# Kernel optimization log

Measured on AMD Instinct MI355X. Metric: run time of the kernel, lower is better.

Reference implementation:

```python
import jax, jax.numpy as jnp
import numpy as np

N, E, H, L, G = 100000, 1000000, 64, 4, 64
D_IN = 2 * H + 3  # edge/coord MLP input: x[row] ++ x[col] ++ rel(3)


def _lin_params(key, fan_in, fan_out):
    kw, kb = jax.random.split(key)
    s = 1.0 / np.sqrt(fan_in)
    w = jax.random.uniform(kw, (fan_in, fan_out), jnp.float32, -s, s)
    b = jax.random.uniform(kb, (fan_out,), jnp.float32, -s, s)
    return w, b


def _stacked(key, fan_in, fan_out, n=L):
    ks = jax.random.split(key, n)
    ws, bs = zip(*[_lin_params(k, fan_in, fan_out) for k in ks])
    return jnp.stack(ws), jnp.stack(bs)


def setup_inputs() -> dict:
    key = jax.random.key(0)
    ks = jax.random.split(key, 16)
    x = jax.random.normal(ks[0], (N, 1), jnp.float32)
    coords = jax.random.normal(ks[1], (N, 3), jnp.float32)
    edge_index = jax.random.randint(ks[2], (2, E), 0, N, jnp.int32)
    batch = jnp.sort(jax.random.randint(ks[3], (N,), 0, G, jnp.int32))
    in_w, in_b = _lin_params(ks[4], 1, H)
    coord_w1, coord_b1 = _stacked(ks[5], D_IN, 2 * H)
    coord_w2, coord_b2 = _stacked(ks[6], 2 * H, 3)
    ew_w, ew_b = _stacked(ks[7], 3, 1)
    cn_scale = jnp.full((L, 1), 0.01, jnp.float32)
    edge_w1, edge_b1 = _stacked(ks[8], D_IN, 2 * H)
    edge_w2, edge_b2 = _stacked(ks[9], 2 * H, H)
    node_w1, node_b1 = _stacked(ks[10], 2 * H, 2 * H)
    node_w2, node_b2 = _stacked(ks[11], 2 * H, H)
    out_w, out_b = _lin_params(ks[12], H, 128)
    return dict(x=x, coords=coords, in_w=in_w, in_b=in_b,
                coord_w1=coord_w1, coord_b1=coord_b1, coord_w2=coord_w2, coord_b2=coord_b2,
                ew_w=ew_w, ew_b=ew_b, cn_scale=cn_scale,
                edge_w1=edge_w1, edge_b1=edge_b1, edge_w2=edge_w2, edge_b2=edge_b2,
                node_w1=node_w1, node_b1=node_b1, node_w2=node_w2, node_b2=node_b2,
                out_w=out_w, out_b=out_b, edge_index=edge_index, batch=batch)


def _layer_norm(h, eps=1e-5):
    mu = jnp.mean(h, -1, keepdims=True)
    var = jnp.var(h, -1, keepdims=True)
    return (h - mu) / jnp.sqrt(var + eps)


def reference(x, coords, in_w, in_b, coord_w1, coord_b1, coord_w2, coord_b2,
              ew_w, ew_b, cn_scale, edge_w1, edge_b1, edge_w2, edge_b2,
              node_w1, node_b1, node_w2, node_b2, out_w, out_b,
              edge_index, batch):
    row, col = edge_index[0], edge_index[1]
    h = x @ in_w + in_b  # [N, H]
    for l in range(L):
        # 1) coord update from OLD coords
        rel = coords[row] - coords[col]                        # [E, 3]
        cin = jnp.concatenate([h[row], h[col], rel], axis=-1)  # [E, 2H+3]
        delta = jax.nn.silu(cin @ coord_w1[l] + coord_b1[l]) @ coord_w2[l] + coord_b2[l]  # [E,3]
        nrm = jnp.maximum(jnp.linalg.norm(delta, axis=-1, keepdims=True), 1e-8)
        delta = delta / nrm * cn_scale[l]                      # CoorsNorm
        delta = delta * jax.nn.sigmoid(rel @ ew_w[l] + ew_b[l])
        coords = coords.at[row].add(delta)
        # 2) edge message / node update from NEW coords
        rel = coords[row] - coords[col]
        ein = jnp.concatenate([h[row], h[col], rel], axis=-1)
        e = jax.nn.silu(jax.nn.silu(ein @ edge_w1[l] + edge_b1[l]) @ edge_w2[l] + edge_b2[l])
        agg = jnp.zeros_like(h).at[row].add(e)                 # scatter-add [N, H]
        nin = jnp.concatenate([h, agg], axis=-1)
        h = h + jax.nn.silu(nin @ node_w1[l] + node_b1[l]) @ node_w2[l] + node_b2[l]
        h = _layer_norm(h)
    # global mean pool
    sums = jax.ops.segment_sum(h, batch, num_segments=G)
    cnts = jax.ops.segment_sum(jnp.ones((h.shape[0], 1), h.dtype), batch, num_segments=G)
    pooled = sums / jnp.maximum(cnts, 1.0)
    out = jax.nn.relu(pooled) @ out_w + out_b                  # [G, 128]
    return out / jnp.maximum(jnp.linalg.norm(out, axis=-1, keepdims=True), 1e-12)
```

## Files before the change

### kernel.cpp

```cpp
#include <hip/hip_runtime.h>
#include <math.h>

#define NN 100000
#define NE 1000000
#define NG 64
#define NL 4
#define NT_E (NE / 32)
#define NT_N (NN / 32)

typedef __attribute__((ext_vector_type(8))) _Float16 f16x8;
typedef __attribute__((ext_vector_type(4))) float f32x4;

#define MFMA16(a, b, c) __builtin_amdgcn_mfma_f32_16x16x32_f16(a, b, c, 0, 0, 0)
#define LOG2E 1.44269504088896340f
__device__ __forceinline__ float fsig_(float x) {
    return __builtin_amdgcn_rcpf(1.0f + __builtin_amdgcn_exp2f(-LOG2E * x));
}
__device__ __forceinline__ float fsilu_(float x) { return x * fsig_(x); }

__global__ void k_init_h(const float* __restrict__ x, const float* __restrict__ in_w,
                         const float* __restrict__ in_b, float* __restrict__ h32,
                         _Float16* __restrict__ h16) {
    int idx = blockIdx.x * blockDim.x + threadIdx.x;
    if (idx >= NN * 64) return;
    int n = idx >> 6, j = idx & 63;
    float v = fmaf(x[n], in_w[j], in_b[j]);
    h32[idx] = v;
    h16[idx] = (_Float16)v;
}

#define SEG0 21504
#define SEG1 21504
#define SEG2 8704
#define SEG3 17408
#define SEG4 8704
#define SEG5 2176
#define SEGTOT (SEG0 + SEG1 + SEG2 + SEG3 + SEG4 + SEG5)
__global__ void k_prep_all(const float* __restrict__ cw1, const float* __restrict__ ew1,
                           const float* __restrict__ ew2, const float* __restrict__ nw1,
                           const float* __restrict__ nw2, const float* __restrict__ cw2,
                           _Float16* __restrict__ cw1T, _Float16* __restrict__ ew1T,
                           _Float16* __restrict__ ew2T, _Float16* __restrict__ nw1T,
                           _Float16* __restrict__ nw2T, _Float16* __restrict__ cw2T) {
    int i = blockIdx.x * blockDim.x + threadIdx.x;
    if (i >= NL * SEGTOT) return;
    int l = i / SEGTOT, r = i - l * SEGTOT;
    const float* src; _Float16* dst; int K, O, SD, j;
    if (r < SEG0) { src = cw1 + (size_t)l * 131 * 128; dst = cw1T + (size_t)l * SEG0; K = 131; O = 128; SD = 168; j = r; }
    else if ((r -= SEG0) < SEG1) { src = ew1 + (size_t)l * 131 * 128; dst = ew1T + (size_t)l * SEG1; K = 131; O = 128; SD = 168; j = r; }
    else if ((r -= SEG1) < SEG2) { src = ew2 + (size_t)l * 128 * 64; dst = ew2T + (size_t)l * SEG2; K = 128; O = 64; SD = 136; j = r; }
    else if ((r -= SEG2) < SEG3) { src = nw1 + (size_t)l * 128 * 128; dst = nw1T + (size_t)l * SEG3; K = 128; O = 128; SD = 136; j = r; }
    else if ((r -= SEG3) < SEG4) { src = nw2 + (size_t)l * 128 * 64; dst = nw2T + (size_t)l * SEG4; K = 128; O = 64; SD = 136; j = r; }
    else {
        r -= SEG4;
        const float* s2 = cw2 + (size_t)l * 128 * 3;
        int o = r / 136, k = r - o * 136;
        cw2T[(size_t)l * SEG5 + r] = (o < 3 && k < 128) ? (_Float16)s2[(size_t)k * 3 + o] : (_Float16)0.0f;
        return;
    }
    int o = j / SD, k = j - o * SD;
    dst[j] = (k < K) ? (_Float16)src[(size_t)k * O + o] : (_Float16)0.0f;
}

__global__ void k_hist(const int* __restrict__ row, int* __restrict__ deg) {
    int e = blockIdx.x * blockDim.x + threadIdx.x;
    if (e < NE) atomicAdd(&deg[row[e]], 1);
}

#define SCB 256
#define SCT 256
#define SCCH ((NN + SCB - 1) / SCB)
__global__ void k_scan_part(const int* __restrict__ deg, int* __restrict__ bsum) {
    __shared__ int red[SCT];
    int b = blockIdx.x;
    int s = b * SCCH, e = min(NN, s + SCCH);
    int sum = 0;
    for (int i = s + threadIdx.x; i < e; i += SCT) sum += deg[i];
    red[threadIdx.x] = sum;
    __syncthreads();
    for (int off = SCT / 2; off > 0; off >>= 1) {
        if (threadIdx.x < off) red[threadIdx.x] += red[threadIdx.x + off];
        __syncthreads();
    }
    if (threadIdx.x == 0) bsum[b] = red[0];
}
__global__ void k_scan_mid(int* __restrict__ bsum) {
    __shared__ int ss[SCB];
    int t = threadIdx.x;
    ss[t] = bsum[t];
    __syncthreads();
    if (t == 0) {
        int run = 0;
        for (int i = 0; i < SCB; ++i) { int v = ss[i]; ss[i] = run; run += v; }
    }
    __syncthreads();
    bsum[t] = ss[t];
}
__global__ void k_scan_fin(const int* __restrict__ deg, const int* __restrict__ bsum,
                           int* __restrict__ rowptr) {
    __shared__ int tsum[SCT];
    int b = blockIdx.x;
    int s = b * SCCH, e = min(NN, s + SCCH);
    const int per = (SCCH + SCT - 1) / SCT;
    int ts = s + threadIdx.x * per;
    int te = min(e, ts + per);
    int sum = 0;
    for (int i = ts; i < te; ++i) sum += deg[i];
    tsum[threadIdx.x] = sum;
    __syncthreads();
    if (threadIdx.x == 0) {
        int run = bsum[b];
        for (int i = 0; i < SCT; ++i) { int v = tsum[i]; tsum[i] = run; run += v; }
    }
    __syncthreads();
    int run = tsum[threadIdx.x];
    for (int i = ts; i < te; ++i) { rowptr[i] = run; run += deg[i]; }
    if (b == 0 && threadIdx.x == 0) rowptr[NN] = NE;
}

__global__ void k_scatter2(const int* __restrict__ row, const int* __restrict__ col,
                           int* __restrict__ pos, int* __restrict__ rowP,
                           int* __restrict__ colP) {
    int e = blockIdx.x * blockDim.x + threadIdx.x;
    if (e < NE) {
        int r = row[e];
        int p = atomicAdd(&pos[r], 1);
        rowP[p] = r;
        colP[p] = col[e];
    }
}

template <int CSR>
__global__ __launch_bounds__(256)
void k_coord3(const _Float16* __restrict__ h16,
              const float* __restrict__ ccur, float* __restrict__ cnext,
              const int* __restrict__ rowP, const int* __restrict__ colP,
              float4* __restrict__ deltas,
              const _Float16* __restrict__ w1T, const float* __restrict__ b1,
              const _Float16* __restrict__ w2T, const float* __restrict__ b2,
              const float* __restrict__ eww, const float* __restrict__ ewb,
              const float* __restrict__ cns) {
    __shared__ __attribute__((aligned(16))) _Float16 cin[32][168];
    __shared__ __attribute__((aligned(16))) _Float16 h1[32][136];
    __shared__ __attribute__((aligned(16))) float pbuf[4][32][17];
    __shared__ float gate[32];
    for (int i = threadIdx.x; i < 32 * 168; i += 256) (&cin[0][0])[i] = (_Float16)0.0f;
    int tid = threadIdx.x;
    int w = tid >> 6, lane = tid & 63, lc = lane & 15, lg = lane >> 4;
    float e0w = eww[0], e1w = eww[1], e2w = eww[2], ebw = ewb[0], sc = cns[0];
    float b20 = b2[0], b21 = b2[1], b22 = b2[2];
    f16x8 bw1[2][5];
#pragma unroll
    for (int ti = 0; ti < 2; ++ti)
#pragma unroll
        for (int ks = 0; ks < 5; ++ks)
            bw1[ti][ks] = *(const f16x8*)&w1T[(size_t)((2 * w + ti) * 16 + lc) * 168 + ks * 32 + lg * 8];
    f16x8 bw2 = *(const f16x8*)&w2T[(size_t)lc * 136 + w * 32 + lg * 8];
    float bias10 = b1[(2 * w) * 16 + lc], bias11 = b1[(2 * w + 1) * 16 + lc];
    __syncthreads();

    for (int tile = blockIdx.x; tile < NT_E; tile += gridDim.x) {
        int e0 = tile * 32;
        {
            int el = tid >> 3, part = tid & 7;
            int r = rowP[e0 + el], c = colP[e0 + el];
            *(f16x8*)&cin[el][part * 8] = *(const f16x8*)&h16[(size_t)r * 64 + part * 8];
            *(f16x8*)&cin[el][64 + part * 8] = *(const f16x8*)&h16[(size_t)c * 64 + part * 8];
        }
        if (tid < 32) {
            int r = rowP[e0 + tid], c = colP[e0 + tid];
            float rx = ccur[r * 3 + 0] - ccur[c * 3 + 0];
            float ry = ccur[r * 3 + 1] - ccur[c * 3 + 1];
            float rz = ccur[r * 3 + 2] - ccur[c * 3 + 2];
            cin[tid][128] = (_Float16)rx; cin[tid][129] = (_Float16)ry; cin[tid][130] = (_Float16)rz;
            gate[tid] = fsig_(fmaf(rx, e0w, fmaf(ry, e1w, fmaf(rz, e2w, ebw))));
        }
        __syncthreads();
        f32x4 acc[2][2];
        acc[0][0] = acc[0][1] = acc[1][0] = acc[1][1] = (f32x4){0.f, 0.f, 0.f, 0.f};
#pragma unroll
        for (int ks = 0; ks < 5; ++ks) {
            f16x8 a0 = *(const f16x8*)&cin[lc][ks * 32 + lg * 8];
            f16x8 a1 = *(const f16x8*)&cin[16 + lc][ks * 32 + lg * 8];
#pragma unroll
            for (int ti = 0; ti < 2; ++ti) {
                acc[0][ti] = MFMA16(a0, bw1[ti][ks], acc[0][ti]);
                acc[1][ti] = MFMA16(a1, bw1[ti][ks], acc[1][ti]);
            }
        }
#pragma unroll
        for (int ti = 0; ti < 2; ++ti) {
            int colc = (2 * w + ti) * 16 + lc;
            float bias = ti ? bias11 : bias10;
#pragma unroll
            for (int rt = 0; rt < 2; ++rt)
#pragma unroll
                for (int j = 0; j < 4; ++j)
                    h1[rt * 16 + lg * 4 + j][colc] = (_Float16)fsilu_(acc[rt][ti][j] + bias);
        }
        __syncthreads();
        f32x4 c2[2];
        c2[0] = c2[1] = (f32x4){0.f, 0.f, 0.f, 0.f};
        {
            f16x8 a0 = *(const f16x8*)&h1[lc][w * 32 + lg * 8];
            f16x8 a1 = *(const f16x8*)&h1[16 + lc][w * 32 + lg * 8];
            c2[0] = MFMA16(a0, bw2, c2[0]);
            c2[1] = MFMA16(a1, bw2, c2[1]);
        }
#pragma unroll
        for (int rt = 0; rt < 2; ++rt)
#pragma unroll
            for (int j = 0; j < 4; ++j)
                pbuf[w][rt * 16 + lg * 4 + j][lc] = c2[rt][j];
        __syncthreads();
        if (tid < 32) {
            float d0 = pbuf[0][tid][0] + pbuf[1][tid][0] + pbuf[2][tid][0] + pbuf[3][tid][0] + b20;
            float d1 = pbuf[0][tid][1] + pbuf[1][tid][1] + pbuf[2][tid][1] + pbuf[3][tid][1] + b21;
            float d2 = pbuf[0][tid][2] + pbuf[1][tid][2] + pbuf[2][tid][2] + pbuf[3][tid][2] + b22;
            float ss = d0 * d0 + d1 * d1 + d2 * d2;
            float nrm = fmaxf(__builtin_amdgcn_sqrtf(ss), 1e-8f);
            float m = sc * __builtin_amdgcn_rcpf(nrm) * gate[tid];
            if (CSR) {
                deltas[e0 + tid] = make_float4(d0 * m, d1 * m, d2 * m, 0.0f);
            } else {
                int r = rowP[e0 + tid];
                atomicAdd(&cnext[(size_t)r * 3 + 0], d0 * m);
                atomicAdd(&cnext[(size_t)r * 3 + 1], d1 * m);
                atomicAdd(&cnext[(size_t)r * 3 + 2], d2 * m);
            }
        }
    }
}

__global__ void k_coord_apply(const float* __restrict__ ccur, float* __restrict__ cnext,
                              const int* __restrict__ rowptr,
                              const float4* __restrict__ deltas) {
    int n = blockIdx.x * blockDim.x + threadIdx.x;
    if (n >= NN) return;
    int s = rowptr[n], e = rowptr[n + 1];
    float d0 = 0.f, d1 = 0.f, d2 = 0.f;
    for (int j = s; j < e; ++j) {
        float4 d = deltas[j];
        d0 += d.x; d1 += d.y; d2 += d.z;
    }
    cnext[(size_t)n * 3 + 0] = ccur[(size_t)n * 3 + 0] + d0;
    cnext[(size_t)n * 3 + 1] = ccur[(size_t)n * 3 + 1] + d1;
    cnext[(size_t)n * 3 + 2] = ccur[(size_t)n * 3 + 2] + d2;
}

template <int CSR>
__global__ __launch_bounds__(256)
void k_edge3(const _Float16* __restrict__ h16, const float* __restrict__ coords,
             float* __restrict__ agg, _Float16* __restrict__ emsgS,
             const int* __restrict__ rowP, const int* __restrict__ colP,
             const _Float16* __restrict__ w1T, const float* __restrict__ b1,
             const _Float16* __restrict__ w2T, const float* __restrict__ b2) {
    __shared__ __attribute__((aligned(16))) _Float16 cin[32][168];
    __shared__ __attribute__((aligned(16))) _Float16 h1[32][136];
    __shared__ __attribute__((aligned(16))) _Float16 msg[32][72];
    for (int i = threadIdx.x; i < 32 * 168; i += 256) (&cin[0][0])[i] = (_Float16)0.0f;
    int tid = threadIdx.x;
    int w = tid >> 6, lane = tid & 63, lc = lane & 15, lg = lane >> 4;
    f16x8 bw1[2][5];
#pragma unroll
    for (int ti = 0; ti < 2; ++ti)
#pragma unroll
        for (int ks = 0; ks < 5; ++ks)
            bw1[ti][ks] = *(const f16x8*)&w1T[(size_t)((2 * w + ti) * 16 + lc) * 168 + ks * 32 + lg * 8];
    f16x8 bw2[4];
#pragma unroll
    for (int ks = 0; ks < 4; ++ks)
        bw2[ks] = *(const f16x8*)&w2T[(size_t)(w * 16 + lc) * 136 + ks * 32 + lg * 8];
    float bias10 = b1[(2 * w) * 16 + lc], bias11 = b1[(2 * w + 1) * 16 + lc];
    float bias2 = b2[w * 16 + lc];
    __syncthreads();

    for (int tile = blockIdx.x; tile < NT_E; tile += gridDim.x) {
        int e0 = tile * 32;
        {
            int el = tid >> 3, part = tid & 7;
            int r = rowP[e0 + el], c = colP[e0 + el];
            *(f16x8*)&cin[el][part * 8] = *(const f16x8*)&h16[(size_t)r * 64 + part * 8];
            *(f16x8*)&cin[el][64 + part * 8] = *(const f16x8*)&h16[(size_t)c * 64 + part * 8];
        }
        if (tid < 32) {
            int r = rowP[e0 + tid], c = colP[e0 + tid];
            cin[tid][128] = (_Float16)(coords[r * 3 + 0] - coords[c * 3 + 0]);
            cin[tid][129] = (_Float16)(coords[r * 3 + 1] - coords[c * 3 + 1]);
            cin[tid][130] = (_Float16)(coords[r * 3 + 2] - coords[c * 3 + 2]);
        }
        __syncthreads();
        f32x4 acc[2][2];
        acc[0][0] = acc[0][1] = acc[1][0] = acc[1][1] = (f32x4){0.f, 0.f, 0.f, 0.f};
#pragma unroll
        for (int ks = 0; ks < 5; ++ks) {
            f16x8 a0 = *(const f16x8*)&cin[lc][ks * 32 + lg * 8];
            f16x8 a1 = *(const f16x8*)&cin[16 + lc][ks * 32 + lg * 8];
#pragma unroll
            for (int ti = 0; ti < 2; ++ti) {
                acc[0][ti] = MFMA16(a0, bw1[ti][ks], acc[0][ti]);
                acc[1][ti] = MFMA16(a1, bw1[ti][ks], acc[1][ti]);
            }
        }
#pragma unroll
        for (int ti = 0; ti < 2; ++ti) {
            int colc = (2 * w + ti) * 16 + lc;
            float bias = ti ? bias11 : bias10;
#pragma unroll
            for (int rt = 0; rt < 2; ++rt)
#pragma unroll
                for (int j = 0; j < 4; ++j)
                    h1[rt * 16 + lg * 4 + j][colc] = (_Float16)fsilu_(acc[rt][ti][j] + bias);
        }
        __syncthreads();
        f32x4 c2[2];
        c2[0] = c2[1] = (f32x4){0.f, 0.f, 0.f, 0.f};
#pragma unroll
        for (int ks = 0; ks < 4; ++ks) {
            f16x8 a0 = *(const f16x8*)&h1[lc][ks * 32 + lg * 8];
            f16x8 a1 = *(const f16x8*)&h1[16 + lc][ks * 32 + lg * 8];
            c2[0] = MFMA16(a0, bw2[ks], c2[0]);
            c2[1] = MFMA16(a1, bw2[ks], c2[1]);
        }
        if (CSR) {
#pragma unroll
            for (int rt = 0; rt < 2; ++rt)
#pragma unroll
                for (int j = 0; j < 4; ++j)
                    msg[rt * 16 + lg * 4 + j][w * 16 + lc] = (_Float16)fsilu_(c2[rt][j] + bias2);
            __syncthreads();
            int r = tid >> 3, part = tid & 7;
            *(f16x8*)&emsgS[(size_t)(e0 + r) * 64 + part * 8] = *(const f16x8*)&msg[r][part * 8];
        } else {
#pragma unroll
            for (int rt = 0; rt < 2; ++rt)
#pragma unroll
                for (int j = 0; j < 4; ++j)
                    atomicAdd(&agg[(size_t)rowP[e0 + rt * 16 + lg * 4 + j] * 64 + w * 16 + lc],
                              fsilu_(c2[rt][j] + bias2));
            __syncthreads();
        }
    }
}

template <int CSR>
__global__ __launch_bounds__(256)
void k_node3(float* __restrict__ h32, _Float16* __restrict__ h16,
             const float* __restrict__ agg, const _Float16* __restrict__ emsgS,
             const int* __restrict__ rowptr,
             const _Float16* __restrict__ w1T, const float* __restrict__ b1,
             const _Float16* __restrict__ w2T, const float* __restrict__ b2) {
    __shared__ __attribute__((aligned(16))) _Float16 cin[32][136];
    __shared__ __attribute__((aligned(16))) _Float16 h1[32][136];
    __shared__ __attribute__((aligned(16))) float vbuf[32][64];
    int tid = threadIdx.x;
    int w = tid >> 6, lane = tid & 63, lc = lane & 15, lg = lane >> 4;
    f16x8 bw1[2][4], bw2[4];
#pragma unroll
    for (int ti = 0; ti < 2; ++ti)
#pragma unroll
        for (int ks = 0; ks < 4; ++ks)
            bw1[ti][ks] = *(const f16x8*)&w1T[(size_t)((2 * w + ti) * 16 + lc) * 136 + ks * 32 + lg * 8];
#pragma unroll
    for (int ks = 0; ks < 4; ++ks)
        bw2[ks] = *(const f16x8*)&w2T[(size_t)(w * 16 + lc) * 136 + ks * 32 + lg * 8];
    float bias10 = b1[(2 * w) * 16 + lc], bias11 = b1[(2 * w + 1) * 16 + lc];
    float bias2 = b2[w * 16 + lc];

    for (int tile = blockIdx.x; tile < NT_N; tile += gridDim.x) {
        int n0 = tile * 32;
        {
            int nl = tid >> 3, part = tid & 7;
            int n = n0 + nl;
            *(f16x8*)&cin[nl][part * 8] = *(const f16x8*)&h16[(size_t)n * 64 + part * 8];
            if (CSR) {
                float a[8] = {0.f, 0.f, 0.f, 0.f, 0.f, 0.f, 0.f, 0.f};
                int s = rowptr[n], e = rowptr[n + 1];
                for (int jj = s; jj < e; ++jj) {
                    f16x8 m = *(const f16x8*)&emsgS[(size_t)jj * 64 + part * 8];
#pragma unroll
                    for (int q = 0; q < 8; ++q) a[q] += (float)m[q];
                }
                f16x8 o;
#pragma unroll
                for (int q = 0; q < 8; ++q) o[q] = (_Float16)a[q];
                *(f16x8*)&cin[nl][64 + part * 8] = o;
            } else {
                f32x4 xx = *(const f32x4*)&agg[(size_t)n * 64 + part * 8];
                f32x4 yy = *(const f32x4*)&agg[(size_t)n * 64 + part * 8 + 4];
                f16x8 o;
                o[0] = (_Float16)xx[0]; o[1] = (_Float16)xx[1]; o[2] = (_Float16)xx[2]; o[3] = (_Float16)xx[3];
                o[4] = (_Float16)yy[0]; o[5] = (_Float16)yy[1]; o[6] = (_Float16)yy[2]; o[7] = (_Float16)yy[3];
                *(f16x8*)&cin[nl][64 + part * 8] = o;
            }
        }
        __syncthreads();
        f32x4 acc[2][2];
        acc[0][0] = acc[0][1] = acc[1][0] = acc[1][1] = (f32x4){0.f, 0.f, 0.f, 0.f};
#pragma unroll
        for (int ks = 0; ks < 4; ++ks) {
            f16x8 a0 = *(const f16x8*)&cin[lc][ks * 32 + lg * 8];
            f16x8 a1 = *(const f16x8*)&cin[16 + lc][ks * 32 + lg * 8];
#pragma unroll
            for (int ti = 0; ti < 2; ++ti) {
                acc[0][ti] = MFMA16(a0, bw1[ti][ks], acc[0][ti]);
                acc[1][ti] = MFMA16(a1, bw1[ti][ks], acc[1][ti]);
            }
        }
#pragma unroll
        for (int ti = 0; ti < 2; ++ti) {
            int colc = (2 * w + ti) * 16 + lc;
            float bias = ti ? bias11 : bias10;
#pragma unroll
            for (int rt = 0; rt < 2; ++rt)
#pragma unroll
                for (int j = 0; j < 4; ++j)
                    h1[rt * 16 + lg * 4 + j][colc] = (_Float16)fsilu_(acc[rt][ti][j] + bias);
        }
        __syncthreads();
        f32x4 c2[2];
        c2[0] = c2[1] = (f32x4){0.f, 0.f, 0.f, 0.f};
#pragma unroll
        for (int ks = 0; ks < 4; ++ks) {
            f16x8 a0 = *(const f16x8*)&h1[lc][ks * 32 + lg * 8];
            f16x8 a1 = *(const f16x8*)&h1[16 + lc][ks * 32 + lg * 8];
            c2[0] = MFMA16(a0, bw2[ks], c2[0]);
            c2[1] = MFMA16(a1, bw2[ks], c2[1]);
        }
#pragma unroll
        for (int rt = 0; rt < 2; ++rt)
#pragma unroll
            for (int j = 0; j < 4; ++j) {
                int rl = rt * 16 + lg * 4 + j, colc = w * 16 + lc;
                vbuf[rl][colc] = h32[(size_t)(n0 + rl) * 64 + colc] + c2[rt][j] + bias2;
            }
        __syncthreads();
        {
            int r = w * 8 + (lane >> 3), sub = lane & 7;
            f32x4 v0 = *(const f32x4*)&vbuf[r][sub * 8];
            f32x4 v1 = *(const f32x4*)&vbuf[r][sub * 8 + 4];
            float s = v0[0] + v0[1] + v0[2] + v0[3] + v1[0] + v1[1] + v1[2] + v1[3];
            float sq = v0[0]*v0[0] + v0[1]*v0[1] + v0[2]*v0[2] + v0[3]*v0[3]
                     + v1[0]*v1[0] + v1[1]*v1[1] + v1[2]*v1[2] + v1[3]*v1[3];
            s += __shfl_xor(s, 1); s += __shfl_xor(s, 2); s += __shfl_xor(s, 4);
            sq += __shfl_xor(sq, 1); sq += __shfl_xor(sq, 2); sq += __shfl_xor(sq, 4);
            float mu = s * (1.0f / 64.0f);
            float var = sq * (1.0f / 64.0f) - mu * mu;
            float rs = __builtin_amdgcn_rcpf(__builtin_amdgcn_sqrtf(var + 1e-5f));
            size_t base = (size_t)(n0 + r) * 64 + sub * 8;
            f32x4 o0, o1; f16x8 oh;
#pragma unroll
            for (int i = 0; i < 4; ++i) {
                o0[i] = (v0[i] - mu) * rs;
                o1[i] = (v1[i] - mu) * rs;
                oh[i] = (_Float16)o0[i];
                oh[4 + i] = (_Float16)o1[i];
            }
            *(f32x4*)&h32[base] = o0;
            *(f32x4*)&h32[base + 4] = o1;
            *(f16x8*)&h16[base] = oh;
        }
        __syncthreads();
    }
}

__global__ void k_pool_seg(const float* __restrict__ h, const int* __restrict__ batch,
                           float* __restrict__ pooled, float* __restrict__ cnt) {
    int lane = threadIdx.x & 63;
    int wid = blockIdx.x * (blockDim.x >> 6) + (threadIdx.x >> 6);
    int nwav = gridDim.x * (blockDim.x >> 6);
    int chunk = (NN + nwav - 1) / nwav;
    int s = wid * chunk;
    if (s >= NN) return;
    int e = s + chunk; if (e > NN) e = NN;
    int g = batch[s];
    float acc = 0.0f, c = 0.0f;
    for (int n = s; n < e; ++n) {
        int b = batch[n];
        if (b != g) {
            atomicAdd(&pooled[g * 64 + lane], acc);
            if (lane == 0) atomicAdd(&cnt[g], c);
            acc = 0.0f; c = 0.0f; g = b;
        }
        acc += h[(size_t)n * 64 + lane];
        c += 1.0f;
    }
    atomicAdd(&pooled[g * 64 + lane], acc);
    if (lane == 0) atomicAdd(&cnt[g], c);
}

__global__ void k_final(const float* __restrict__ pooled, const float* __restrict__ cnt,
                        const float* __restrict__ ow, const float* __restrict__ ob,
                        float* __restrict__ out) {
    __shared__ float red[2];
    int g = blockIdx.x, o = threadIdx.x;
    float c = fmaxf(cnt[g], 1.0f);
    float acc = ob[o];
#pragma unroll
    for (int j = 0; j < 64; ++j) {
        float pm = fmaxf(pooled[g * 64 + j] / c, 0.0f);
        acc = fmaf(pm, ow[j * 128 + o], acc);
    }
    float ss = acc * acc;
#pragma unroll
    for (int off = 32; off > 0; off >>= 1) ss += __shfl_xor(ss, off);
    if ((o & 63) == 0) red[o >> 6] = ss;
    __syncthreads();
    float nrm = sqrtf(red[0] + red[1]);
    out[g * 128 + o] = acc / fmaxf(nrm, 1e-12f);
}

extern "C" void kernel_launch(void* const* d_in, const int* in_sizes, int n_in,
                              void* d_out, int out_size, void* d_ws, size_t ws_size,
                              hipStream_t stream) {
    const float* x         = (const float*)d_in[0];
    const float* coords_in = (const float*)d_in[1];
    const float* in_w      = (const float*)d_in[2];
    const float* in_b      = (const float*)d_in[3];
    const float* coord_w1  = (const float*)d_in[4];
    const float* coord_b1  = (const float*)d_in[5];
    const float* coord_w2  = (const float*)d_in[6];
    const float* coord_b2  = (const float*)d_in[7];
    const float* ew_w      = (const float*)d_in[8];
    const float* ew_b      = (const float*)d_in[9];
    const float* cn_scale  = (const float*)d_in[10];
    const float* edge_w1   = (const float*)d_in[11];
    const float* edge_b1   = (const float*)d_in[12];
    const float* edge_w2   = (const float*)d_in[13];
    const float* edge_b2   = (const float*)d_in[14];
    const float* node_w1   = (const float*)d_in[15];
    const float* node_b1   = (const float*)d_in[16];
    const float* node_w2   = (const float*)d_in[17];
    const float* node_b2   = (const float*)d_in[18];
    const float* out_w     = (const float*)d_in[19];
    const float* out_b     = (const float*)d_in[20];
    const int* ei          = (const int*)d_in[21];
    const int* batch       = (const int*)d_in[22];
    const int* row = ei;
    const int* col = ei + NE;

    char* wp = (char*)d_ws;
    float* h32    = (float*)wp; wp += (size_t)NN * 64 * 4;
    float* cA     = (float*)wp; wp += (size_t)NN * 3 * 4;
    float* cB     = (float*)wp; wp += (size_t)NN * 3 * 4;
    float* pooled = (float*)wp; wp += (size_t)NG * 64 * 4;
    float* cnt    = (float*)wp; wp += (size_t)NG * 4;
    _Float16* h16  = (_Float16*)wp; wp += (size_t)NN * 64 * 2;
    _Float16* cw1T = (_Float16*)wp; wp += (size_t)NL * SEG0 * 2;
    _Float16* ew1T = (_Float16*)wp; wp += (size_t)NL * SEG1 * 2;
    _Float16* ew2T = (_Float16*)wp; wp += (size_t)NL * SEG2 * 2;
    _Float16* nw1T = (_Float16*)wp; wp += (size_t)NL * SEG3 * 2;
    _Float16* nw2T = (_Float16*)wp; wp += (size_t)NL * SEG4 * 2;
    _Float16* cw2T = (_Float16*)wp; wp += (size_t)NL * SEG5 * 2;
    int* deg       = (int*)wp;            wp += (size_t)NN * 4;
    int* rowptr    = (int*)wp;            wp += (size_t)(NN + 4) * 4;
    int* pos       = (int*)wp;            wp += (size_t)NN * 4;
    int* bsum      = (int*)wp;            wp += (size_t)SCB * 4;
    int* rowP      = (int*)wp;            wp += (size_t)NE * 4;
    int* colP      = (int*)wp;            wp += (size_t)NE * 4;
    float4* deltas = (float4*)wp;         wp += (size_t)NE * 16;
    _Float16* emsgS= (_Float16*)wp;       wp += (size_t)NE * 64 * 2;
    size_t csr_need = (size_t)(wp - (char*)d_ws);
    float* agg = (float*)deg;
    bool use_csr = (ws_size >= csr_need);

    if (use_csr) {
        hipMemsetAsync(deg, 0, (size_t)NN * 4, stream);
        k_hist<<<(NE + 255) / 256, 256, 0, stream>>>(row, deg);
        k_scan_part<<<SCB, SCT, 0, stream>>>(deg, bsum);
        k_scan_mid<<<1, SCB, 0, stream>>>(bsum);
        k_scan_fin<<<SCB, SCT, 0, stream>>>(deg, bsum, rowptr);
        hipMemcpyAsync(pos, rowptr, (size_t)NN * 4, hipMemcpyDeviceToDevice, stream);
        k_scatter2<<<(NE + 255) / 256, 256, 0, stream>>>(row, col, pos, rowP, colP);
    }
    k_prep_all<<<(NL * SEGTOT + 255) / 256, 256, 0, stream>>>(
        coord_w1, edge_w1, edge_w2, node_w1, node_w2, coord_w2,
        cw1T, ew1T, ew2T, nw1T, nw2T, cw2T);
    k_init_h<<<(NN * 64 + 255) / 256, 256, 0, stream>>>(x, in_w, in_b, h32, h16);

    const float* cur = coords_in;
    float* nxt = cA;
    for (int l = 0; l < NL; ++l) {
        if (use_csr) {
            k_coord3<1><<<2048, 256, 0, stream>>>(h16, cur, nullptr, rowP, colP, deltas,
                cw1T + (size_t)l * SEG0, coord_b1 + l * 128,
                cw2T + (size_t)l * SEG5, coord_b2 + l * 3,
                ew_w + l * 3, ew_b + l, cn_scale + l);
            k_coord_apply<<<(NN + 255) / 256, 256, 0, stream>>>(cur, nxt, rowptr, deltas);
            k_edge3<1><<<2048, 256, 0, stream>>>(h16, nxt, nullptr, emsgS, rowP, colP,
                ew1T + (size_t)l * SEG1, edge_b1 + l * 128,
                ew2T + (size_t)l * SEG2, edge_b2 + l * 64);
            k_node3<1><<<1024, 256, 0, stream>>>(h32, h16, nullptr, emsgS, rowptr,
                nw1T + (size_t)l * SEG3, node_b1 + l * 128,
                nw2T + (size_t)l * SEG4, node_b2 + l * 64);
        } else {
            hipMemcpyAsync(nxt, cur, (size_t)NN * 3 * sizeof(float), hipMemcpyDeviceToDevice, stream);
            k_coord3<0><<<2048, 256, 0, stream>>>(h16, cur, nxt, row, col, nullptr,
                cw1T + (size_t)l * SEG0, coord_b1 + l * 128,
                cw2T + (size_t)l * SEG5, coord_b2 + l * 3,
                ew_w + l * 3, ew_b + l, cn_scale + l);
            hipMemsetAsync(agg, 0, (size_t)NN * 64 * 4, stream);
            k_edge3<0><<<2048, 256, 0, stream>>>(h16, nxt, agg, nullptr, row, col,
                ew1T + (size_t)l * SEG1, edge_b1 + l * 128,
                ew2T + (size_t)l * SEG2, edge_b2 + l * 64);
            k_node3<0><<<1024, 256, 0, stream>>>(h32, h16, agg, nullptr, nullptr,
                nw1T + (size_t)l * SEG3, node_b1 + l * 128,
                nw2T + (size_t)l * SEG4, node_b2 + l * 64);
        }
        cur = nxt;
        nxt = (nxt == cA) ? cB : cA;
    }
    hipMemsetAsync(pooled, 0, (size_t)(NG * 64 + NG) * sizeof(float), stream);
    k_pool_seg<<<512, 256, 0, stream>>>(h32, batch, pooled, cnt);
    k_final<<<NG, 128, 0, stream>>>(pooled, cnt, out_w, out_b, (float*)d_out);
}
```

Measured before the change: 1.196 ms.

## Fuse edge message MLP and node update into one per-node-block kernel

```diff
diff --git a/kernel.cpp b/kernel.cpp
--- a/kernel.cpp
+++ b/kernel.cpp
@@ -66,7 +66,6 @@
     int e = blockIdx.x * blockDim.x + threadIdx.x;
     if (e < NE) atomicAdd(&deg[row[e]], 1);
 }
-
 #define SCB 256
 #define SCT 256
 #define SCCH ((NN + SCB - 1) / SCB)
@@ -117,7 +116,6 @@
     for (int i = ts; i < te; ++i) { rowptr[i] = run; run += deg[i]; }
     if (b == 0 && threadIdx.x == 0) rowptr[NN] = NE;
 }
-
 __global__ void k_scatter2(const int* __restrict__ row, const int* __restrict__ col,
                            int* __restrict__ pos, int* __restrict__ rowP,
                            int* __restrict__ colP) {
@@ -248,46 +246,63 @@
     cnext[(size_t)n * 3 + 2] = ccur[(size_t)n * 3 + 2] + d2;
 }
 
-template <int CSR>
 __global__ __launch_bounds__(256)
-void k_edge3(const _Float16* __restrict__ h16, const float* __restrict__ coords,
-             float* __restrict__ agg, _Float16* __restrict__ emsgS,
-             const int* __restrict__ rowP, const int* __restrict__ colP,
-             const _Float16* __restrict__ w1T, const float* __restrict__ b1,
-             const _Float16* __restrict__ w2T, const float* __restrict__ b2) {
+void k_edge_node(const _Float16* __restrict__ h16cur, const float* __restrict__ h32cur,
+                 _Float16* __restrict__ h16nxt, float* __restrict__ h32nxt,
+                 const float* __restrict__ coords,
+                 const int* __restrict__ rowP, const int* __restrict__ colP,
+                 const int* __restrict__ rowptr,
+                 const _Float16* __restrict__ ew1T, const float* __restrict__ eb1,
+                 const _Float16* __restrict__ ew2T, const float* __restrict__ eb2,
+                 const _Float16* __restrict__ nw1T, const float* __restrict__ nb1,
+                 const _Float16* __restrict__ nw2T, const float* __restrict__ nb2) {
     __shared__ __attribute__((aligned(16))) _Float16 cin[32][168];
     __shared__ __attribute__((aligned(16))) _Float16 h1[32][136];
     __shared__ __attribute__((aligned(16))) _Float16 msg[32][72];
-    for (int i = threadIdx.x; i < 32 * 168; i += 256) (&cin[0][0])[i] = (_Float16)0.0f;
+    __shared__ __attribute__((aligned(16))) float aggL[32][64];
+    __shared__ int lrL[32];
     int tid = threadIdx.x;
     int w = tid >> 6, lane = tid & 63, lc = lane & 15, lg = lane >> 4;
+    int n0 = blockIdx.x * 32;
+
+    for (int i = tid; i < 32 * 168; i += 256) (&cin[0][0])[i] = (_Float16)0.0f;
+    for (int i = tid; i < 32 * 64; i += 256) (&aggL[0][0])[i] = 0.0f;
+
     f16x8 bw1[2][5];
 #pragma unroll
     for (int ti = 0; ti < 2; ++ti)
 #pragma unroll
         for (int ks = 0; ks < 5; ++ks)
-            bw1[ti][ks] = *(const f16x8*)&w1T[(size_t)((2 * w + ti) * 16 + lc) * 168 + ks * 32 + lg * 8];
+            bw1[ti][ks] = *(const f16x8*)&ew1T[(size_t)((2 * w + ti) * 16 + lc) * 168 + ks * 32 + lg * 8];
     f16x8 bw2[4];
 #pragma unroll
     for (int ks = 0; ks < 4; ++ks)
-        bw2[ks] = *(const f16x8*)&w2T[(size_t)(w * 16 + lc) * 136 + ks * 32 + lg * 8];
-    float bias10 = b1[(2 * w) * 16 + lc], bias11 = b1[(2 * w + 1) * 16 + lc];
-    float bias2 = b2[w * 16 + lc];
-    __syncthreads();
-
-    for (int tile = blockIdx.x; tile < NT_E; tile += gridDim.x) {
-        int e0 = tile * 32;
+        bw2[ks] = *(const f16x8*)&ew2T[(size_t)(w * 16 + lc) * 136 + ks * 32 + lg * 8];
+    float ebias10 = eb1[(2 * w) * 16 + lc], ebias11 = eb1[(2 * w + 1) * 16 + lc];
+    float ebias2 = eb2[w * 16 + lc];
+    __syncthreads();
+
+    int eBeg = rowptr[n0], eEnd = rowptr[n0 + 32];
+    for (int e0 = eBeg; e0 < eEnd; e0 += 32) {
+        int nval = min(32, eEnd - e0);
         {
             int el = tid >> 3, part = tid & 7;
-            int r = rowP[e0 + el], c = colP[e0 + el];
-            *(f16x8*)&cin[el][part * 8] = *(const f16x8*)&h16[(size_t)r * 64 + part * 8];
-            *(f16x8*)&cin[el][64 + part * 8] = *(const f16x8*)&h16[(size_t)c * 64 + part * 8];
-        }
-        if (tid < 32) {
-            int r = rowP[e0 + tid], c = colP[e0 + tid];
-            cin[tid][128] = (_Float16)(coords[r * 3 + 0] - coords[c * 3 + 0]);
-            cin[tid][129] = (_Float16)(coords[r * 3 + 1] - coords[c * 3 + 1]);
-            cin[tid][130] = (_Float16)(coords[r * 3 + 2] - coords[c * 3 + 2]);
+            if (el < nval) {
+                int r = rowP[e0 + el], c = colP[e0 + el];
+                *(f16x8*)&cin[el][part * 8] = *(const f16x8*)&h16cur[(size_t)r * 64 + part * 8];
+                *(f16x8*)&cin[el][64 + part * 8] = *(const f16x8*)&h16cur[(size_t)c * 64 + part * 8];
+            }
+            if (tid < 32) {
+                if (tid < nval) {
+                    int r = rowP[e0 + tid], c = colP[e0 + tid];
+                    cin[tid][128] = (_Float16)(coords[r * 3 + 0] - coords[c * 3 + 0]);
+                    cin[tid][129] = (_Float16)(coords[r * 3 + 1] - coords[c * 3 + 1]);
+                    cin[tid][130] = (_Float16)(coords[r * 3 + 2] - coords[c * 3 + 2]);
+                    lrL[tid] = rowP[e0 + tid] - n0;
+                } else {
+                    lrL[tid] = -1;
+                }
+            }
         }
         __syncthreads();
         f32x4 acc[2][2];
@@ -305,7 +320,7 @@
 #pragma unroll
         for (int ti = 0; ti < 2; ++ti) {
             int colc = (2 * w + ti) * 16 + lc;
-            float bias = ti ? bias11 : bias10;
+            float bias = ti ? ebias11 : ebias10;
 #pragma unroll
             for (int rt = 0; rt < 2; ++rt)
 #pragma unroll
@@ -322,34 +337,208 @@
             c2[0] = MFMA16(a0, bw2[ks], c2[0]);
             c2[1] = MFMA16(a1, bw2[ks], c2[1]);
         }
-        if (CSR) {
+#pragma unroll
+        for (int rt = 0; rt < 2; ++rt)
+#pragma unroll
+            for (int j = 0; j < 4; ++j)
+                msg[rt * 16 + lg * 4 + j][w * 16 + lc] = (_Float16)fsilu_(c2[rt][j] + ebias2);
+        __syncthreads();
+        {
+            int colj = tid & 63, stripe = tid >> 6;
+            int r0 = stripe * 8;
+            float a = 0.0f;
+            int prev = -1;
+            for (int r = r0; r < r0 + 8; ++r) {
+                if (r >= nval) break;
+                int lr = lrL[r];
+                if (lr != prev) {
+                    if (prev >= 0) atomicAdd(&aggL[prev][colj], a);
+                    a = 0.0f; prev = lr;
+                }
+                a += (float)msg[r][colj];
+            }
+            if (prev >= 0) atomicAdd(&aggL[prev][colj], a);
+        }
+        __syncthreads();
+    }
+
+    f16x8 nbw1[2][4], nbw2[4];
+#pragma unroll
+    for (int ti = 0; ti < 2; ++ti)
+#pragma unroll
+        for (int ks = 0; ks < 4; ++ks)
+            nbw1[ti][ks] = *(const f16x8*)&nw1T[(size_t)((2 * w + ti) * 16 + lc) * 136 + ks * 32 + lg * 8];
+#pragma unroll
+    for (int ks = 0; ks < 4; ++ks)
+        nbw2[ks] = *(const f16x8*)&nw2T[(size_t)(w * 16 + lc) * 136 + ks * 32 + lg * 8];
+    float nbias10 = nb1[(2 * w) * 16 + lc], nbias11 = nb1[(2 * w + 1) * 16 + lc];
+    float nbias2 = nb2[w * 16 + lc];
+    {
+        int nl = tid >> 3, part = tid & 7;
+        int n = n0 + nl;
+        *(f16x8*)&cin[nl][part * 8] = *(const f16x8*)&h16cur[(size_t)n * 64 + part * 8];
+        f32x4 xx = *(const f32x4*)&aggL[nl][part * 8];
+        f32x4 yy = *(const f32x4*)&aggL[nl][part * 8 + 4];
+        f16x8 o;
+        o[0] = (_Float16)xx[0]; o[1] = (_Float16)xx[1]; o[2] = (_Float16)xx[2]; o[3] = (_Float16)xx[3];
+        o[4] = (_Float16)yy[0]; o[5] = (_Float16)yy[1]; o[6] = (_Float16)yy[2]; o[7] = (_Float16)yy[3];
+        *(f16x8*)&cin[nl][64 + part * 8] = o;
+    }
+    __syncthreads();
+    f32x4 acc[2][2];
+    acc[0][0] = acc[0][1] = acc[1][0] = acc[1][1] = (f32x4){0.f, 0.f, 0.f, 0.f};
+#pragma unroll
+    for (int ks = 0; ks < 4; ++ks) {
+        f16x8 a0 = *(const f16x8*)&cin[lc][ks * 32 + lg * 8];
+        f16x8 a1 = *(const f16x8*)&cin[16 + lc][ks * 32 + lg * 8];
+#pragma unroll
+        for (int ti = 0; ti < 2; ++ti) {
+            acc[0][ti] = MFMA16(a0, nbw1[ti][ks], acc[0][ti]);
+            acc[1][ti] = MFMA16(a1, nbw1[ti][ks], acc[1][ti]);
+        }
+    }
+#pragma unroll
+    for (int ti = 0; ti < 2; ++ti) {
+        int colc = (2 * w + ti) * 16 + lc;
+        float bias = ti ? nbias11 : nbias10;
+#pragma unroll
+        for (int rt = 0; rt < 2; ++rt)
+#pragma unroll
+            for (int j = 0; j < 4; ++j)
+                h1[rt * 16 + lg * 4 + j][colc] = (_Float16)fsilu_(acc[rt][ti][j] + bias);
+    }
+    __syncthreads();
+    f32x4 c2[2];
+    c2[0] = c2[1] = (f32x4){0.f, 0.f, 0.f, 0.f};
+#pragma unroll
+    for (int ks = 0; ks < 4; ++ks) {
+        f16x8 a0 = *(const f16x8*)&h1[lc][ks * 32 + lg * 8];
+        f16x8 a1 = *(const f16x8*)&h1[16 + lc][ks * 32 + lg * 8];
+        c2[0] = MFMA16(a0, nbw2[ks], c2[0]);
+        c2[1] = MFMA16(a1, nbw2[ks], c2[1]);
+    }
+    float (*vbuf)[64] = (float(*)[64])&cin[0][0];
+#pragma unroll
+    for (int rt = 0; rt < 2; ++rt)
+#pragma unroll
+        for (int j = 0; j < 4; ++j) {
+            int rl = rt * 16 + lg * 4 + j, colc = w * 16 + lc;
+            vbuf[rl][colc] = h32cur[(size_t)(n0 + rl) * 64 + colc] + c2[rt][j] + nbias2;
+        }
+    __syncthreads();
+    {
+        int r = w * 8 + (lane >> 3), sub = lane & 7;
+        f32x4 v0 = *(const f32x4*)&vbuf[r][sub * 8];
+        f32x4 v1 = *(const f32x4*)&vbuf[r][sub * 8 + 4];
+        float s = v0[0] + v0[1] + v0[2] + v0[3] + v1[0] + v1[1] + v1[2] + v1[3];
+        float sq = v0[0]*v0[0] + v0[1]*v0[1] + v0[2]*v0[2] + v0[3]*v0[3]
+                 + v1[0]*v1[0] + v1[1]*v1[1] + v1[2]*v1[2] + v1[3]*v1[3];
+        s += __shfl_xor(s, 1); s += __shfl_xor(s, 2); s += __shfl_xor(s, 4);
+        sq += __shfl_xor(sq, 1); sq += __shfl_xor(sq, 2); sq += __shfl_xor(sq, 4);
+        float mu = s * (1.0f / 64.0f);
+        float var = sq * (1.0f / 64.0f) - mu * mu;
+        float rs = __builtin_amdgcn_rcpf(__builtin_amdgcn_sqrtf(var + 1e-5f));
+        size_t base = (size_t)(n0 + r) * 64 + sub * 8;
+        f32x4 o0, o1; f16x8 oh;
+#pragma unroll
+        for (int i = 0; i < 4; ++i) {
+            o0[i] = (v0[i] - mu) * rs;
+            o1[i] = (v1[i] - mu) * rs;
+            oh[i] = (_Float16)o0[i];
+            oh[4 + i] = (_Float16)o1[i];
+        }
+        *(f32x4*)&h32nxt[base] = o0;
+        *(f32x4*)&h32nxt[base + 4] = o1;
+        *(f16x8*)&h16nxt[base] = oh;
+    }
+}
+
+__global__ __launch_bounds__(256)
+void k_edge_legacy(const _Float16* __restrict__ h16, const float* __restrict__ coords,
+                   float* __restrict__ agg,
+                   const int* __restrict__ row, const int* __restrict__ col,
+                   const _Float16* __restrict__ w1T, const float* __restrict__ b1,
+                   const _Float16* __restrict__ w2T, const float* __restrict__ b2) {
+    __shared__ __attribute__((aligned(16))) _Float16 cin[32][168];
+    __shared__ __attribute__((aligned(16))) _Float16 h1[32][136];
+    for (int i = threadIdx.x; i < 32 * 168; i += 256) (&cin[0][0])[i] = (_Float16)0.0f;
+    int tid = threadIdx.x;
+    int w = tid >> 6, lane = tid & 63, lc = lane & 15, lg = lane >> 4;
+    f16x8 bw1[2][5];
+#pragma unroll
+    for (int ti = 0; ti < 2; ++ti)
+#pragma unroll
+        for (int ks = 0; ks < 5; ++ks)
+            bw1[ti][ks] = *(const f16x8*)&w1T[(size_t)((2 * w + ti) * 16 + lc) * 168 + ks * 32 + lg * 8];
+    f16x8 bw2[4];
+#pragma unroll
+    for (int ks = 0; ks < 4; ++ks)
+        bw2[ks] = *(const f16x8*)&w2T[(size_t)(w * 16 + lc) * 136 + ks * 32 + lg * 8];
+    float bias10 = b1[(2 * w) * 16 + lc], bias11 = b1[(2 * w + 1) * 16 + lc];
+    float bias2 = b2[w * 16 + lc];
+    __syncthreads();
+    for (int tile = blockIdx.x; tile < NT_E; tile += gridDim.x) {
+        int e0 = tile * 32;
+        {
+            int el = tid >> 3, part = tid & 7;
+            int r = row[e0 + el], c = col[e0 + el];
+            *(f16x8*)&cin[el][part * 8] = *(const f16x8*)&h16[(size_t)r * 64 + part * 8];
+            *(f16x8*)&cin[el][64 + part * 8] = *(const f16x8*)&h16[(size_t)c * 64 + part * 8];
+        }
+        if (tid < 32) {
+            int r = row[e0 + tid], c = col[e0 + tid];
+            cin[tid][128] = (_Float16)(coords[r * 3 + 0] - coords[c * 3 + 0]);
+            cin[tid][129] = (_Float16)(coords[r * 3 + 1] - coords[c * 3 + 1]);
+            cin[tid][130] = (_Float16)(coords[r * 3 + 2] - coords[c * 3 + 2]);
+        }
+        __syncthreads();
+        f32x4 acc[2][2];
+        acc[0][0] = acc[0][1] = acc[1][0] = acc[1][1] = (f32x4){0.f, 0.f, 0.f, 0.f};
+#pragma unroll
+        for (int ks = 0; ks < 5; ++ks) {
+            f16x8 a0 = *(const f16x8*)&cin[lc][ks * 32 + lg * 8];
+            f16x8 a1 = *(const f16x8*)&cin[16 + lc][ks * 32 + lg * 8];
+#pragma unroll
+            for (int ti = 0; ti < 2; ++ti) {
+                acc[0][ti] = MFMA16(a0, bw1[ti][ks], acc[0][ti]);
+                acc[1][ti] = MFMA16(a1, bw1[ti][ks], acc[1][ti]);
+            }
+        }
+#pragma unroll
+        for (int ti = 0; ti < 2; ++ti) {
+            int colc = (2 * w + ti) * 16 + lc;
+            float bias = ti ? bias11 : bias10;
 #pragma unroll
             for (int rt = 0; rt < 2; ++rt)
 #pragma unroll
                 for (int j = 0; j < 4; ++j)
-                    msg[rt * 16 + lg * 4 + j][w * 16 + lc] = (_Float16)fsilu_(c2[rt][j] + bias2);
-            __syncthreads();
-            int r = tid >> 3, part = tid & 7;
-            *(f16x8*)&emsgS[(size_t)(e0 + r) * 64 + part * 8] = *(const f16x8*)&msg[r][part * 8];
-        } else {
-#pragma unroll
-            for (int rt = 0; rt < 2; ++rt)
-#pragma unroll
-                for (int j = 0; j < 4; ++j)
-                    atomicAdd(&agg[(size_t)rowP[e0 + rt * 16 + lg * 4 + j] * 64 + w * 16 + lc],
-                              fsilu_(c2[rt][j] + bias2));
-            __syncthreads();
-        }
-    }
-}
-
-template <int CSR>
+                    h1[rt * 16 + lg * 4 + j][colc] = (_Float16)fsilu_(acc[rt][ti][j] + bias);
+        }
+        __syncthreads();
+        f32x4 c2[2];
+        c2[0] = c2[1] = (f32x4){0.f, 0.f, 0.f, 0.f};
+#pragma unroll
+        for (int ks = 0; ks < 4; ++ks) {
+            f16x8 a0 = *(const f16x8*)&h1[lc][ks * 32 + lg * 8];
+            f16x8 a1 = *(const f16x8*)&h1[16 + lc][ks * 32 + lg * 8];
+            c2[0] = MFMA16(a0, bw2[ks], c2[0]);
+            c2[1] = MFMA16(a1, bw2[ks], c2[1]);
+        }
+#pragma unroll
+        for (int rt = 0; rt < 2; ++rt)
+#pragma unroll
+            for (int j = 0; j < 4; ++j)
+                atomicAdd(&agg[(size_t)row[e0 + rt * 16 + lg * 4 + j] * 64 + w * 16 + lc],
+                          fsilu_(c2[rt][j] + bias2));
+        __syncthreads();
+    }
+}
+
 __global__ __launch_bounds__(256)
-void k_node3(float* __restrict__ h32, _Float16* __restrict__ h16,
-             const float* __restrict__ agg, const _Float16* __restrict__ emsgS,
-             const int* __restrict__ rowptr,
-             const _Float16* __restrict__ w1T, const float* __restrict__ b1,
-             const _Float16* __restrict__ w2T, const float* __restrict__ b2) {
+void k_node_legacy(float* __restrict__ h32, _Float16* __restrict__ h16,
+                   const float* __restrict__ agg,
+                   const _Float16* __restrict__ w1T, const float* __restrict__ b1,
+                   const _Float16* __restrict__ w2T, const float* __restrict__ b2) {
     __shared__ __attribute__((aligned(16))) _Float16 cin[32][136];
     __shared__ __attribute__((aligned(16))) _Float16 h1[32][136];
     __shared__ __attribute__((aligned(16))) float vbuf[32][64];
@@ -366,33 +555,18 @@
         bw2[ks] = *(const f16x8*)&w2T[(size_t)(w * 16 + lc) * 136 + ks * 32 + lg * 8];
     float bias10 = b1[(2 * w) * 16 + lc], bias11 = b1[(2 * w + 1) * 16 + lc];
     float bias2 = b2[w * 16 + lc];
-
     for (int tile = blockIdx.x; tile < NT_N; tile += gridDim.x) {
         int n0 = tile * 32;
         {
             int nl = tid >> 3, part = tid & 7;
             int n = n0 + nl;
             *(f16x8*)&cin[nl][part * 8] = *(const f16x8*)&h16[(size_t)n * 64 + part * 8];
-            if (CSR) {
-                float a[8] = {0.f, 0.f, 0.f, 0.f, 0.f, 0.f, 0.f, 0.f};
-                int s = rowptr[n], e = rowptr[n + 1];
-                for (int jj = s; jj < e; ++jj) {
-                    f16x8 m = *(const f16x8*)&emsgS[(size_t)jj * 64 + part * 8];
-#pragma unroll
-                    for (int q = 0; q < 8; ++q) a[q] += (float)m[q];
-                }
-                f16x8 o;
-#pragma unroll
-                for (int q = 0; q < 8; ++q) o[q] = (_Float16)a[q];
-                *(f16x8*)&cin[nl][64 + part * 8] = o;
-            } else {
-                f32x4 xx = *(const f32x4*)&agg[(size_t)n * 64 + part * 8];
-                f32x4 yy = *(const f32x4*)&agg[(size_t)n * 64 + part * 8 + 4];
-                f16x8 o;
-                o[0] = (_Float16)xx[0]; o[1] = (_Float16)xx[1]; o[2] = (_Float16)xx[2]; o[3] = (_Float16)xx[3];
-                o[4] = (_Float16)yy[0]; o[5] = (_Float16)yy[1]; o[6] = (_Float16)yy[2]; o[7] = (_Float16)yy[3];
-                *(f16x8*)&cin[nl][64 + part * 8] = o;
-            }
+            f32x4 xx = *(const f32x4*)&agg[(size_t)n * 64 + part * 8];
+            f32x4 yy = *(const f32x4*)&agg[(size_t)n * 64 + part * 8 + 4];
+            f16x8 o;
+            o[0] = (_Float16)xx[0]; o[1] = (_Float16)xx[1]; o[2] = (_Float16)xx[2]; o[3] = (_Float16)xx[3];
+            o[4] = (_Float16)yy[0]; o[5] = (_Float16)yy[1]; o[6] = (_Float16)yy[2]; o[7] = (_Float16)yy[3];
+            *(f16x8*)&cin[nl][64 + part * 8] = o;
         }
         __syncthreads();
         f32x4 acc[2][2];
@@ -540,26 +714,27 @@
     const int* col = ei + NE;
 
     char* wp = (char*)d_ws;
-    float* h32    = (float*)wp; wp += (size_t)NN * 64 * 4;
+    float* h32A   = (float*)wp; wp += (size_t)NN * 64 * 4;
+    float* h32B   = (float*)wp; wp += (size_t)NN * 64 * 4;
     float* cA     = (float*)wp; wp += (size_t)NN * 3 * 4;
     float* cB     = (float*)wp; wp += (size_t)NN * 3 * 4;
     float* pooled = (float*)wp; wp += (size_t)NG * 64 * 4;
     float* cnt    = (float*)wp; wp += (size_t)NG * 4;
-    _Float16* h16  = (_Float16*)wp; wp += (size_t)NN * 64 * 2;
+    _Float16* h16A = (_Float16*)wp; wp += (size_t)NN * 64 * 2;
+    _Float16* h16B = (_Float16*)wp; wp += (size_t)NN * 64 * 2;
     _Float16* cw1T = (_Float16*)wp; wp += (size_t)NL * SEG0 * 2;
     _Float16* ew1T = (_Float16*)wp; wp += (size_t)NL * SEG1 * 2;
     _Float16* ew2T = (_Float16*)wp; wp += (size_t)NL * SEG2 * 2;
     _Float16* nw1T = (_Float16*)wp; wp += (size_t)NL * SEG3 * 2;
     _Float16* nw2T = (_Float16*)wp; wp += (size_t)NL * SEG4 * 2;
     _Float16* cw2T = (_Float16*)wp; wp += (size_t)NL * SEG5 * 2;
-    int* deg       = (int*)wp;            wp += (size_t)NN * 4;
-    int* rowptr    = (int*)wp;            wp += (size_t)(NN + 4) * 4;
-    int* pos       = (int*)wp;            wp += (size_t)NN * 4;
-    int* bsum      = (int*)wp;            wp += (size_t)SCB * 4;
-    int* rowP      = (int*)wp;            wp += (size_t)NE * 4;
-    int* colP      = (int*)wp;            wp += (size_t)NE * 4;
-    float4* deltas = (float4*)wp;         wp += (size_t)NE * 16;
-    _Float16* emsgS= (_Float16*)wp;       wp += (size_t)NE * 64 * 2;
+    int* deg       = (int*)wp;    wp += (size_t)NN * 4;
+    int* rowptr    = (int*)wp;    wp += (size_t)(NN + 4) * 4;
+    int* pos       = (int*)wp;    wp += (size_t)NN * 4;
+    int* bsum      = (int*)wp;    wp += (size_t)SCB * 4;
+    int* rowP      = (int*)wp;    wp += (size_t)NE * 4;
+    int* colP      = (int*)wp;    wp += (size_t)NE * 4;
+    float4* deltas = (float4*)wp; wp += (size_t)NE * 16;
     size_t csr_need = (size_t)(wp - (char*)d_ws);
     float* agg = (float*)deg;
     bool use_csr = (ws_size >= csr_need);
@@ -576,41 +751,47 @@
     k_prep_all<<<(NL * SEGTOT + 255) / 256, 256, 0, stream>>>(
         coord_w1, edge_w1, edge_w2, node_w1, node_w2, coord_w2,
         cw1T, ew1T, ew2T, nw1T, nw2T, cw2T);
-    k_init_h<<<(NN * 64 + 255) / 256, 256, 0, stream>>>(x, in_w, in_b, h32, h16);
-
-    const float* cur = coords_in;
-    float* nxt = cA;
+    k_init_h<<<(NN * 64 + 255) / 256, 256, 0, stream>>>(x, in_w, in_b, h32A, h16A);
+
+    const float* c_cur = coords_in;
+    float* c_nxt = cA;
+    float* h32cur = h32A; float* h32nxt = h32B;
+    _Float16* h16cur = h16A; _Float16* h16nxt = h16B;
+
     for (int l = 0; l < NL; ++l) {
         if (use_csr) {
-            k_coord3<1><<<2048, 256, 0, stream>>>(h16, cur, nullptr, rowP, colP, deltas,
+            k_coord3<1><<<2048, 256, 0, stream>>>(h16cur, c_cur, nullptr, rowP, colP, deltas,
                 cw1T + (size_t)l * SEG0, coord_b1 + l * 128,
                 cw2T + (size_t)l * SEG5, coord_b2 + l * 3,
                 ew_w + l * 3, ew_b + l, cn_scale + l);
-            k_coord_apply<<<(NN + 255) / 256, 256, 0, stream>>>(cur, nxt, rowptr, deltas);
-            k_edge3<1><<<2048, 256, 0, stream>>>(h16, nxt, nullptr, emsgS, rowP, colP,
+            k_coord_apply<<<(NN + 255) / 256, 256, 0, stream>>>(c_cur, c_nxt, rowptr, deltas);
+            k_edge_node<<<NT_N, 256, 0, stream>>>(h16cur, h32cur, h16nxt, h32nxt, c_nxt,
+                rowP, colP, rowptr,
                 ew1T + (size_t)l * SEG1, edge_b1 + l * 128,
-                ew2T + (size_t)l * SEG2, edge_b2 + l * 64);
-            k_node3<1><<<1024, 256, 0, stream>>>(h32, h16, nullptr, emsgS, rowptr,
+                ew2T + (size_t)l * SEG2, edge_b2 + l * 64,
                 nw1T + (size_t)l * SEG3, node_b1 + l * 128,
                 nw2T + (size_t)l * SEG4, node_b2 + l * 64);
+            { float* t = h32cur; h32cur = h32nxt; h32nxt = t; }
+            { _Float16* t = h16cur; h16cur = h16nxt; h16nxt = t; }
         } else {
-            hipMemcpyAsync(nxt, cur, (size_t)NN * 3 * sizeof(float), hipMemcpyDeviceToDevice, stream);
-            k_coord3<0><<<2048, 256, 0, stream>>>(h16, cur, nxt, row, col, nullptr,
+            hipMemcpyAsync(c_nxt, c_cur, (size_t)NN * 3 * sizeof(float), hipMemcpyDeviceToDevice, stream);
+            k_coord3<0><<<2048, 256, 0, stream>>>(h16A, c_cur, c_nxt, row, col, nullptr,
                 cw1T + (size_t)l * SEG0, coord_b1 + l * 128,
                 cw2T + (size_t)l * SEG5, coord_b2 + l * 3,
                 ew_w + l * 3, ew_b + l, cn_scale + l);
             hipMemsetAsync(agg, 0, (size_t)NN * 64 * 4, stream);
-            k_edge3<0><<<2048, 256, 0, stream>>>(h16, nxt, agg, nullptr, row, col,
+            k_edge_legacy<<<2048, 256, 0, stream>>>(h16A, c_nxt, agg, row, col,
                 ew1T + (size_t)l * SEG1, edge_b1 + l * 128,
                 ew2T + (size_t)l * SEG2, edge_b2 + l * 64);
-            k_node3<0><<<1024, 256, 0, stream>>>(h32, h16, agg, nullptr, nullptr,
+            k_node_legacy<<<1024, 256, 0, stream>>>(h32A, h16A, agg,
                 nw1T + (size_t)l * SEG3, node_b1 + l * 128,
                 nw2T + (size_t)l * SEG4, node_b2 + l * 64);
         }
-        cur = nxt;
-        nxt = (nxt == cA) ? cB : cA;
-    }
+        { const float* t = c_cur; c_cur = c_nxt; c_nxt = (t == cA || t == coords_in) ? ((c_nxt == cA) ? cB : cA) : (float*)t; }
+        if (c_nxt == c_cur) c_nxt = (c_cur == cA) ? cB : cA;
+    }
+    const float* hfinal = use_csr ? h32cur : h32A;
     hipMemsetAsync(pooled, 0, (size_t)(NG * 64 + NG) * sizeof(float), stream);
-    k_pool_seg<<<512, 256, 0, stream>>>(h32, batch, pooled, cnt);
+    k_pool_seg<<<512, 256, 0, stream>>>(hfinal, batch, pooled, cnt);
     k_final<<<NG, 128, 0, stream>>>(pooled, cnt, out_w, out_b, (float*)d_out);
 }
```

Result: slower. 1.461 ms (+22.1%).
